# Performance work log

Hardware: AMD Instinct MI355X
Metric: run time of the kernel (lower is better)

Reference implementation:

```python
import jax, jax.numpy as jnp
import numpy as np

N = 50000
E = 800000
IN = 256
HID = 64
H12 = 4
LAT = 32
NEG_SLOPE = 0.2


def gat_conv(x, src, dst, W, a_src, a_dst, b, heads, out_ch, concat):
    """PyG GATConv (eval mode, add_self_loops already applied to src/dst).
    x: [N, F_in]; src/dst: [Etot]; W: [F_in, heads*out_ch]; a_*: [heads, out_ch]; b: bias.
    Returns (out, alpha[Etot, heads])."""
    n = x.shape[0]
    h = (x @ W).reshape(n, heads, out_ch)                 # [N,H,C]
    e_src = (h * a_src).sum(-1)                           # [N,H]
    e_dst = (h * a_dst).sum(-1)                           # [N,H]
    e = jax.nn.leaky_relu(e_src[src] + e_dst[dst], NEG_SLOPE)   # [Etot,H]
    emax = jax.ops.segment_max(e, dst, num_segments=n)
    ee = jnp.exp(e - emax[dst])
    denom = jax.ops.segment_sum(ee, dst, num_segments=n)
    alpha = ee / (denom[dst] + 1e-16)                     # segment softmax over incoming edges
    msg = h[src] * alpha[:, :, None]                      # [Etot,H,C]
    out = jax.ops.segment_sum(msg, dst, num_segments=n)   # [N,H,C]
    out = out.reshape(n, heads * out_ch) if concat else out.mean(axis=1)
    return out + b, alpha


def setup_inputs() -> dict:
    key = jax.random.key(0)
    ks = jax.random.split(key, 20)
    s = 0.1
    inp = {
        "x": jax.random.normal(ks[0], (N, IN), jnp.float32),
        "edge_index": jax.random.randint(ks[1], (2, E), 0, N, jnp.int32),
        "W1": jax.random.normal(ks[2], (IN, H12 * HID), jnp.float32) * s,
        "a1s": jax.random.normal(ks[3], (H12, HID), jnp.float32) * s,
        "a1d": jax.random.normal(ks[4], (H12, HID), jnp.float32) * s,
        "b1": jnp.zeros((H12 * HID,), jnp.float32),
        "W2": jax.random.normal(ks[5], (H12 * HID, H12 * HID), jnp.float32) * s,
        "a2s": jax.random.normal(ks[6], (H12, HID), jnp.float32) * s,
        "a2d": jax.random.normal(ks[7], (H12, HID), jnp.float32) * s,
        "b2": jnp.zeros((HID,), jnp.float32),
        "Wm": jax.random.normal(ks[8], (HID, LAT), jnp.float32) * s,
        "ams": jax.random.normal(ks[9], (1, LAT), jnp.float32) * s,
        "amd": jax.random.normal(ks[10], (1, LAT), jnp.float32) * s,
        "bm": jnp.zeros((LAT,), jnp.float32),
        # log_std head
        "Ws": jax.random.normal(ks[11], (HID, LAT), jnp.float32) * s,
        "ass": jax.random.normal(ks[12], (1, LAT), jnp.float32) * s,
        "asd": jax.random.normal(ks[13], (1, LAT), jnp.float32) * s,
        "bs": jnp.zeros((LAT,), jnp.float32),
    }
    return inp


def reference(x, edge_index, W1, a1s, a1d, b1, W2, a2s, a2d, b2,
              Wm, ams, amd, bm, Ws, ass, asd, bs):
    # GATConv adds self loops by default
    loops = jnp.arange(N, dtype=edge_index.dtype)
    src = jnp.concatenate([edge_index[0], loops])
    dst = jnp.concatenate([edge_index[1], loops])

    h1, a_w1 = gat_conv(x, src, dst, W1, a1s, a1d, b1, H12, HID, True)
    h1 = jax.nn.relu(h1)
    h2, a_w2 = gat_conv(h1, src, dst, W2, a2s, a2d, b2, H12, HID, False)
    h2 = jax.nn.relu(h2)  # dropout is identity in eval mode
    z_mean, a_wm = gat_conv(h2, src, dst, Wm, ams, amd, bm, 1, LAT, False)
    z_log_std, a_ws = gat_conv(h2, src, dst, Ws, ass, asd, bs, 1, LAT, False)
    return (z_mean, z_log_std, a_w1, a_w2, a_wm, a_ws)
```

## Files before the change

kernel.cpp:

```cpp
#include <hip/hip_runtime.h>
#include <cstdint>
#include <cstddef>

#define NN 50000
#define EE 800000
#define ETOT 850000
#define NEG_SLOPE 0.2f

typedef _Float16 f16;
typedef __attribute__((ext_vector_type(4))) _Float16 f16x4;
typedef __attribute__((ext_vector_type(8))) _Float16 f16x8;
typedef __attribute__((ext_vector_type(4))) float f32x4;


__global__ __launch_bounds__(256) void deg_kernel(const int* __restrict__ ei, int* __restrict__ deg) {
    int e = blockIdx.x * 256 + threadIdx.x;
    if (e >= ETOT) return;
    int d = (e < EE) ? ei[EE + e] : (e - EE);
    atomicAdd(&deg[d], 1);
}

__global__ __launch_bounds__(256) void scan1_kernel(const int* __restrict__ deg, int* __restrict__ offs,
                                                    int* __restrict__ bsum, int n) {
    __shared__ int sh[256];
    int i = blockIdx.x * 256 + threadIdx.x;
    int v = (i < n) ? deg[i] : 0;
    sh[threadIdx.x] = v;
    __syncthreads();
    for (int off = 1; off < 256; off <<= 1) {
        int t = (threadIdx.x >= off) ? sh[threadIdx.x - off] : 0;
        __syncthreads();
        sh[threadIdx.x] += t;
        __syncthreads();
    }
    if (i < n) offs[i] = sh[threadIdx.x] - v;
    if (threadIdx.x == 255) bsum[blockIdx.x] = sh[255];
}

__global__ __launch_bounds__(256) void scan2_kernel(int* __restrict__ bsum, int nb) {
    __shared__ int sh[256];
    int v = (threadIdx.x < nb) ? bsum[threadIdx.x] : 0;
    sh[threadIdx.x] = v;
    __syncthreads();
    for (int off = 1; off < 256; off <<= 1) {
        int t = (threadIdx.x >= off) ? sh[threadIdx.x - off] : 0;
        __syncthreads();
        sh[threadIdx.x] += t;
        __syncthreads();
    }
    if (threadIdx.x < nb) bsum[threadIdx.x] = sh[threadIdx.x] - v;
}

__global__ __launch_bounds__(256) void scan3_kernel(const int* __restrict__ bsum, int* __restrict__ offs,
                                                    int* __restrict__ cursor, int n) {
    int i = blockIdx.x * 256 + threadIdx.x;
    if (i < n) {
        int o = offs[i] + bsum[blockIdx.x];
        offs[i] = o;
        cursor[i] = o;
    }
}

__global__ __launch_bounds__(256) void fill_kernel(const int* __restrict__ ei, int* __restrict__ cursor,
                                                   int* __restrict__ csrc) {
    int e = blockIdx.x * 256 + threadIdx.x;
    if (e >= ETOT) return;
    int d, s;
    if (e < EE) { s = ei[e]; d = ei[EE + e]; } else { s = e - EE; d = e - EE; }
    int p = atomicAdd(&cursor[d], 1);
    csrc[p] = s;
}


template<int K, bool AF32>
__global__ __launch_bounds__(256) void mfma_gemm(const void* __restrict__ Ap, const f16* __restrict__ Bt,
                                                 f16* __restrict__ C, int M, int N) {
    int w = threadIdx.x >> 6, lane = threadIdx.x & 63;
    int m0 = blockIdx.y * 128 + w * 32;
    int n0 = blockIdx.x * 64;
    int r = lane & 15, kb = lane >> 4;
    int ar0 = m0 + r;       if (ar0 > M - 1) ar0 = M - 1;
    int ar1 = m0 + 16 + r;  if (ar1 > M - 1) ar1 = M - 1;
    f32x4 acc[2][4] = {};
    const float* Af = (const float*)Ap;
    const f16*   Ah = (const f16*)Ap;
    size_t a0off = (size_t)ar0 * K + kb * 8;
    size_t a1off = (size_t)ar1 * K + kb * 8;
    const f16* bbase = Bt + (size_t)(n0 + r) * K + kb * 8;
    for (int k0 = 0; k0 < K; k0 += 32) {
        f16x8 a0, a1;
        if constexpr (AF32) {
            float4 l0 = *(const float4*)(Af + a0off + k0);
            float4 h0 = *(const float4*)(Af + a0off + k0 + 4);
            float4 l1 = *(const float4*)(Af + a1off + k0);
            float4 h1 = *(const float4*)(Af + a1off + k0 + 4);
            a0[0]=(f16)l0.x; a0[1]=(f16)l0.y; a0[2]=(f16)l0.z; a0[3]=(f16)l0.w;
            a0[4]=(f16)h0.x; a0[5]=(f16)h0.y; a0[6]=(f16)h0.z; a0[7]=(f16)h0.w;
            a1[0]=(f16)l1.x; a1[1]=(f16)l1.y; a1[2]=(f16)l1.z; a1[3]=(f16)l1.w;
            a1[4]=(f16)h1.x; a1[5]=(f16)h1.y; a1[6]=(f16)h1.z; a1[7]=(f16)h1.w;
        } else {
            a0 = *(const f16x8*)(Ah + a0off + k0);
            a1 = *(const f16x8*)(Ah + a1off + k0);
        }
#pragma unroll
        for (int ni = 0; ni < 4; ++ni) {
            f16x8 b = *(const f16x8*)(bbase + (size_t)ni * 16 * K + k0);
            acc[0][ni] = __builtin_amdgcn_mfma_f32_16x16x32_f16(a0, b, acc[0][ni], 0, 0, 0);
            acc[1][ni] = __builtin_amdgcn_mfma_f32_16x16x32_f16(a1, b, acc[1][ni], 0, 0, 0);
        }
    }
#pragma unroll
    for (int mi = 0; mi < 2; ++mi) {
#pragma unroll
        for (int i = 0; i < 4; ++i) {
            int row = m0 + mi * 16 + kb * 4 + i;
            if (row < M) {
#pragma unroll
                for (int ni = 0; ni < 4; ++ni)
                    C[(size_t)row * N + n0 + ni * 16 + r] = (f16)acc[mi][ni][i];
            }
        }
    }
}


__global__ __launch_bounds__(256) void packw_kernel(const float* __restrict__ W1, const float* __restrict__ W2,
                                                    const float* __restrict__ Wm, const float* __restrict__ Ws,
                                                    const float* __restrict__ ams, const float* __restrict__ ass,
                                                    const float* __restrict__ amd, const float* __restrict__ asd,
                                                    f16* __restrict__ Wt1, f16* __restrict__ Wt2,
                                                    f16* __restrict__ Wtms,
                                                    float* __restrict__ aS, float* __restrict__ aD) {
    int i = blockIdx.x * 256 + threadIdx.x;
    if (i < 65536) {
        int n = i >> 8, k = i & 255;
        Wt1[(size_t)n * 256 + k] = (f16)W1[(size_t)k * 256 + n];
        Wt2[(size_t)n * 256 + k] = (f16)W2[(size_t)k * 256 + n];
    }
    if (i < 4096) {
        int c = i >> 6, k = i & 63;
        float v = (c < 32) ? Wm[k * 32 + c] : Ws[k * 32 + (c - 32)];
        Wtms[(size_t)c * 64 + k] = (f16)v;
    }
    if (i < 64) {
        aS[i] = (i < 32) ? ams[i] : ass[i - 32];
        aD[i] = (i < 32) ? amd[i] : asd[i - 32];
    }
}


__global__ __launch_bounds__(256) void scores4_kernel(const f16* __restrict__ H, const float* __restrict__ aS,
                                                      const float* __restrict__ aD, float* __restrict__ es,
                                                      float* __restrict__ ed) {
    int wave = threadIdx.x >> 6, lane = threadIdx.x & 63;
    int n = blockIdx.x * 4 + wave;
    if (n >= NN) return;
    f16x4 h = *(const f16x4*)(H + (size_t)n * 256 + lane * 4);
    float4 s4 = *(const float4*)(aS + lane * 4);
    float4 d4 = *(const float4*)(aD + lane * 4);
    float hx = (float)h[0], hy = (float)h[1], hz = (float)h[2], hw = (float)h[3];
    float ps = hx * s4.x + hy * s4.y + hz * s4.z + hw * s4.w;
    float pd = hx * d4.x + hy * d4.y + hz * d4.z + hw * d4.w;
    for (int off = 1; off < 16; off <<= 1) { ps += __shfl_xor(ps, off); pd += __shfl_xor(pd, off); }
    if ((lane & 15) == 0) {
        int hh = lane >> 4;
        es[n * 4 + hh] = ps;
        ed[n * 4 + hh] = pd;
    }
}

__global__ __launch_bounds__(256) void scores_ms_kernel(const f16* __restrict__ H, const float* __restrict__ aS,
                                                        const float* __restrict__ aD, float* __restrict__ es,
                                                        float* __restrict__ ed) {
    int wave = threadIdx.x >> 6, lane = threadIdx.x & 63;
    int n = blockIdx.x * 4 + wave;
    if (n >= NN) return;
    float h = (float)H[(size_t)n * 64 + lane];
    float ps = h * aS[lane];
    float pd = h * aD[lane];
    for (int off = 1; off < 32; off <<= 1) { ps += __shfl_xor(ps, off); pd += __shfl_xor(pd, off); }
    if ((lane & 31) == 0) {
        int g = lane >> 5;
        es[n * 2 + g] = ps;
        ed[n * 2 + g] = pd;
    }
}

__device__ __forceinline__ float leaky(float v) { return v > 0.f ? v : NEG_SLOPE * v; }


__global__ __launch_bounds__(256) void alpha4_kernel(const int* __restrict__ ei, const float* __restrict__ es,
                                                     const float* __restrict__ ed, const float* __restrict__ inv,
                                                     float* __restrict__ out4) {
    int e = blockIdx.x * 256 + threadIdx.x;
    if (e >= ETOT) return;
    int s, d;
    if (e < EE) { s = ei[e]; d = ei[EE + e]; } else { s = e - EE; d = e - EE; }
    float4 esv = *(const float4*)(es + (size_t)s * 4);
    float4 edv = *(const float4*)(ed + (size_t)d * 4);
    float4 iv  = *(const float4*)(inv + (size_t)d * 4);
    float4 r;
    r.x = __expf(leaky(esv.x + edv.x)) * iv.x;
    r.y = __expf(leaky(esv.y + edv.y)) * iv.y;
    r.z = __expf(leaky(esv.z + edv.z)) * iv.z;
    r.w = __expf(leaky(esv.w + edv.w)) * iv.w;
    *(float4*)(out4 + (size_t)e * 4) = r;
}

__global__ __launch_bounds__(256) void alpha_ms_kernel(const int* __restrict__ ei, const float* __restrict__ es,
                                                       const float* __restrict__ ed, const float* __restrict__ inv,
                                                       float* __restrict__ awm, float* __restrict__ aws) {
    int e = blockIdx.x * 256 + threadIdx.x;
    if (e >= ETOT) return;
    int s, d;
    if (e < EE) { s = ei[e]; d = ei[EE + e]; } else { s = e - EE; d = e - EE; }
    float2 esv = *(const float2*)(es + (size_t)s * 2);
    float2 edv = *(const float2*)(ed + (size_t)d * 2);
    float2 iv  = *(const float2*)(inv + (size_t)d * 2);
    awm[e] = __expf(leaky(esv.x + edv.x)) * iv.x;
    aws[e] = __expf(leaky(esv.y + edv.y)) * iv.y;
}


__global__ __launch_bounds__(128) void agg_concat_kernel(
    const f16* __restrict__ H, const float* __restrict__ es, const float* __restrict__ ed,
    const int* __restrict__ offs, const int* __restrict__ csrc,
    const float* __restrict__ bias, f16* __restrict__ out, float* __restrict__ invout) {
    int wave = threadIdx.x >> 6, lane = threadIdx.x & 63;
    int n = blockIdx.x * 2 + wave;
    if (n >= NN) return;
    int start = offs[n];
    int end = (n + 1 < NN) ? offs[n + 1] : ETOT;
    int deg = end - start;
    int h16 = lane >> 4, sub = lane & 15;
    float edh = ed[n * 4 + h16];
    float dsum = 0.f;
    for (int j = sub; j < deg; j += 16) {
        int s = csrc[start + j];
        dsum += __expf(leaky(es[s * 4 + h16] + edh));
    }
    for (int off = 1; off < 16; off <<= 1) dsum += __shfl_xor(dsum, off);
    float inv = 1.f / (dsum + 1e-16f);
    if (sub == 0) invout[n * 4 + h16] = inv;
    int half = lane >> 5;
    int l5 = lane & 31;
    int hh = l5 >> 3;
    int c8 = l5 * 8;
    float invh = __shfl(inv, hh << 4);
    float edhh = __shfl(edh, hh << 4);
    float accv[8] = {};
    int j = half;
    for (; j + 6 < deg; j += 8) {
        int p0 = start + j, p1 = start + j + 2, p2 = start + j + 4, p3 = start + j + 6;
        int s0 = csrc[p0], s1 = csrc[p1], s2 = csrc[p2], s3 = csrc[p3];
        float a0 = __expf(leaky(es[s0 * 4 + hh] + edhh)) * invh;
        float a1 = __expf(leaky(es[s1 * 4 + hh] + edhh)) * invh;
        float a2 = __expf(leaky(es[s2 * 4 + hh] + edhh)) * invh;
        float a3 = __expf(leaky(es[s3 * 4 + hh] + edhh)) * invh;
        f16x8 v0 = *(const f16x8*)(H + (size_t)s0 * 256 + c8);
        f16x8 v1 = *(const f16x8*)(H + (size_t)s1 * 256 + c8);
        f16x8 v2 = *(const f16x8*)(H + (size_t)s2 * 256 + c8);
        f16x8 v3 = *(const f16x8*)(H + (size_t)s3 * 256 + c8);
#pragma unroll
        for (int k = 0; k < 8; ++k)
            accv[k] += a0 * (float)v0[k] + a1 * (float)v1[k] + a2 * (float)v2[k] + a3 * (float)v3[k];
    }
    for (; j < deg; j += 2) {
        int p0 = start + j;
        int s0 = csrc[p0];
        float a0 = __expf(leaky(es[s0 * 4 + hh] + edhh)) * invh;
        f16x8 v0 = *(const f16x8*)(H + (size_t)s0 * 256 + c8);
#pragma unroll
        for (int k = 0; k < 8; ++k) accv[k] += a0 * (float)v0[k];
    }
#pragma unroll
    for (int k = 0; k < 8; ++k) accv[k] += __shfl_xor(accv[k], 32);
    if (lane < 32) {
        f16x8 r;
#pragma unroll
        for (int k = 0; k < 8; ++k) r[k] = (f16)fmaxf(accv[k] + bias[c8 + k], 0.f);
        *(f16x8*)(out + (size_t)n * 256 + c8) = r;
    }
}


__global__ __launch_bounds__(128) void agg_mean_kernel(
    const f16* __restrict__ H, const float* __restrict__ es, const float* __restrict__ ed,
    const int* __restrict__ offs, const int* __restrict__ csrc,
    const float* __restrict__ bias, f16* __restrict__ out, float* __restrict__ invout) {
    int wave = threadIdx.x >> 6, lane = threadIdx.x & 63;
    int n = blockIdx.x * 2 + wave;
    if (n >= NN) return;
    int start = offs[n];
    int end = (n + 1 < NN) ? offs[n + 1] : ETOT;
    int deg = end - start;
    int h16 = lane >> 4, sub = lane & 15;
    float edh = ed[n * 4 + h16];
    float dsum = 0.f;
    for (int j = sub; j < deg; j += 16) {
        int s = csrc[start + j];
        dsum += __expf(leaky(es[s * 4 + h16] + edh));
    }
    for (int off = 1; off < 16; off <<= 1) dsum += __shfl_xor(dsum, off);
    float inv = 1.f / (dsum + 1e-16f);
    if (sub == 0) invout[n * 4 + h16] = inv;
    int half = lane >> 5;
    int l5 = lane & 31;
    int hh = l5 >> 3;
    int c8 = l5 * 8;
    float invh = __shfl(inv, hh << 4);
    float edhh = __shfl(edh, hh << 4);
    float accv[8] = {};
    int j = half;
    for (; j + 6 < deg; j += 8) {
        int p0 = start + j, p1 = start + j + 2, p2 = start + j + 4, p3 = start + j + 6;
        int s0 = csrc[p0], s1 = csrc[p1], s2 = csrc[p2], s3 = csrc[p3];
        float a0 = __expf(leaky(es[s0 * 4 + hh] + edhh)) * invh;
        float a1 = __expf(leaky(es[s1 * 4 + hh] + edhh)) * invh;
        float a2 = __expf(leaky(es[s2 * 4 + hh] + edhh)) * invh;
        float a3 = __expf(leaky(es[s3 * 4 + hh] + edhh)) * invh;
        f16x8 v0 = *(const f16x8*)(H + (size_t)s0 * 256 + c8);
        f16x8 v1 = *(const f16x8*)(H + (size_t)s1 * 256 + c8);
        f16x8 v2 = *(const f16x8*)(H + (size_t)s2 * 256 + c8);
        f16x8 v3 = *(const f16x8*)(H + (size_t)s3 * 256 + c8);
#pragma unroll
        for (int k = 0; k < 8; ++k)
            accv[k] += a0 * (float)v0[k] + a1 * (float)v1[k] + a2 * (float)v2[k] + a3 * (float)v3[k];
    }
    for (; j < deg; j += 2) {
        int p0 = start + j;
        int s0 = csrc[p0];
        float a0 = __expf(leaky(es[s0 * 4 + hh] + edhh)) * invh;
        f16x8 v0 = *(const f16x8*)(H + (size_t)s0 * 256 + c8);
#pragma unroll
        for (int k = 0; k < 8; ++k) accv[k] += a0 * (float)v0[k];
    }
#pragma unroll
    for (int k = 0; k < 8; ++k) {
        accv[k] += __shfl_xor(accv[k], 8);
        accv[k] += __shfl_xor(accv[k], 16);
        accv[k] += __shfl_xor(accv[k], 32);
    }
    if (lane < 8) {
        f16x8 r;
#pragma unroll
        for (int k = 0; k < 8; ++k) r[k] = (f16)fmaxf(accv[k] * 0.25f + bias[lane * 8 + k], 0.f);
        *(f16x8*)(out + (size_t)n * 64 + lane * 8) = r;
    }
}


__global__ __launch_bounds__(128) void agg_ms_kernel(
    const f16* __restrict__ H, const float* __restrict__ es, const float* __restrict__ ed,
    const int* __restrict__ offs, const int* __restrict__ csrc,
    const float* __restrict__ bm, const float* __restrict__ bs,
    float* __restrict__ zmean, float* __restrict__ zlog, float* __restrict__ invout) {
    int wave = threadIdx.x >> 6, lane = threadIdx.x & 63;
    int n = blockIdx.x * 2 + wave;
    if (n >= NN) return;
    int start = offs[n];
    int end = (n + 1 < NN) ? offs[n + 1] : ETOT;
    int deg = end - start;
    int g = lane >> 5, sub = lane & 31;
    float edg = ed[n * 2 + g];
    float dsum = 0.f;
    for (int j = sub; j < deg; j += 32) {
        int s = csrc[start + j];
        dsum += __expf(leaky(es[s * 2 + g] + edg));
    }
    for (int off = 1; off < 32; off <<= 1) dsum += __shfl_xor(dsum, off);
    float inv = 1.f / (dsum + 1e-16f);
    if (sub == 0) invout[n * 2 + g] = inv;
    int slot = lane >> 3;
    int le = lane & 7;
    int g2 = le >> 2;
    int c8 = le * 8;
    float invg = __shfl(inv, g2 << 5);
    float edg2 = __shfl(edg, g2 << 5);
    float accv[8] = {};
    for (int j = slot; j < deg; j += 8) {
        int p = start + j;
        int s = csrc[p];
        float a = __expf(leaky(es[s * 2 + g2] + edg2)) * invg;
        f16x8 v = *(const f16x8*)(H + (size_t)s * 64 + c8);
#pragma unroll
        for (int k = 0; k < 8; ++k) accv[k] += a * (float)v[k];
    }
#pragma unroll
    for (int k = 0; k < 8; ++k) {
        accv[k] += __shfl_xor(accv[k], 8);
        accv[k] += __shfl_xor(accv[k], 16);
        accv[k] += __shfl_xor(accv[k], 32);
    }
    if (lane < 4) {
        float4 r0, r1;
        int cb = lane * 8;
        r0.x = accv[0] + bm[cb + 0]; r0.y = accv[1] + bm[cb + 1];
        r0.z = accv[2] + bm[cb + 2]; r0.w = accv[3] + bm[cb + 3];
        r1.x = accv[4] + bm[cb + 4]; r1.y = accv[5] + bm[cb + 5];
        r1.z = accv[6] + bm[cb + 6]; r1.w = accv[7] + bm[cb + 7];
        *(float4*)(zmean + (size_t)n * 32 + cb) = r0;
        *(float4*)(zmean + (size_t)n * 32 + cb + 4) = r1;
    } else if (lane < 8) {
        float4 r0, r1;
        int cb = (lane - 4) * 8;
        r0.x = accv[0] + bs[cb + 0]; r0.y = accv[1] + bs[cb + 1];
        r0.z = accv[2] + bs[cb + 2]; r0.w = accv[3] + bs[cb + 3];
        r1.x = accv[4] + bs[cb + 4]; r1.y = accv[5] + bs[cb + 5];
        r1.z = accv[6] + bs[cb + 6]; r1.w = accv[7] + bs[cb + 7];
        *(float4*)(zlog + (size_t)n * 32 + cb) = r0;
        *(float4*)(zlog + (size_t)n * 32 + cb + 4) = r1;
    }
}


extern "C" void kernel_launch(void* const* d_in, const int* in_sizes, int n_in,
                              void* d_out, int out_size, void* d_ws, size_t ws_size,
                              hipStream_t stream) {
    const float* x   = (const float*)d_in[0];
    const int*   ei  = (const int*)d_in[1];
    const float* W1  = (const float*)d_in[2];
    const float* a1s = (const float*)d_in[3];
    const float* a1d = (const float*)d_in[4];
    const float* b1  = (const float*)d_in[5];
    const float* W2  = (const float*)d_in[6];
    const float* a2s = (const float*)d_in[7];
    const float* a2d = (const float*)d_in[8];
    const float* b2  = (const float*)d_in[9];
    const float* Wm  = (const float*)d_in[10];
    const float* ams = (const float*)d_in[11];
    const float* amd = (const float*)d_in[12];
    const float* bm  = (const float*)d_in[13];
    const float* Ws  = (const float*)d_in[14];
    const float* ass = (const float*)d_in[15];
    const float* asd = (const float*)d_in[16];
    const float* bs  = (const float*)d_in[17];

    float* out = (float*)d_out;
    float* zmean = out;
    float* zlog  = out + 1600000;
    float* a_w1  = out + 3200000;
    float* a_w2  = out + 6600000;
    float* a_wm  = out + 10000000;
    float* a_ws_o = out + 10850000;

    float* ws = (float*)d_ws;
    size_t o = 0;
    f16*   Hh   = (f16*)(ws + o); o += (size_t)NN * 128;
    f16*   h1h  = (f16*)(ws + o); o += (size_t)NN * 128;
    f16*   h2h  = (f16*)(ws + o); o += (size_t)NN * 32;
    float* es1  = ws + o; o += NN * 4;
    float* ed1  = ws + o; o += NN * 4;
    float* es2  = ws + o; o += NN * 4;
    float* ed2  = ws + o; o += NN * 4;
    float* esms = ws + o; o += NN * 2;
    float* edms = ws + o; o += NN * 2;
    float* inv1 = ws + o; o += NN * 4;
    float* inv2 = ws + o; o += NN * 4;
    float* invms= ws + o; o += NN * 2;
    f16*   Wt1  = (f16*)(ws + o); o += 32768;
    f16*   Wt2  = (f16*)(ws + o); o += 32768;
    f16*   Wtms = (f16*)(ws + o); o += 2048;
    float* aSms = ws + o; o += 64;
    float* aDms = ws + o; o += 64;
    int* deg    = (int*)(ws + o); o += NN;
    int* offs   = (int*)(ws + o); o += NN;
    int* cursor = (int*)(ws + o); o += NN;
    int* csrc   = (int*)(ws + o); o += ETOT;

    const int edgeBlocks = (ETOT + 255) / 256;
    const int nodeBlocks = (NN + 255) / 256;
    const int waveBlocks = (NN + 3) / 4;
    const int aggBlocks  = (NN + 1) / 2;

    hipMemsetAsync(deg, 0, NN * sizeof(int), stream);
    deg_kernel<<<edgeBlocks, 256, 0, stream>>>(ei, deg);
    scan1_kernel<<<nodeBlocks, 256, 0, stream>>>(deg, offs, cursor , NN);
    scan2_kernel<<<1, 256, 0, stream>>>(cursor, nodeBlocks);
    scan3_kernel<<<nodeBlocks, 256, 0, stream>>>(cursor, offs, deg , NN);
    fill_kernel<<<edgeBlocks, 256, 0, stream>>>(ei, deg, csrc);

    packw_kernel<<<256, 256, 0, stream>>>(W1, W2, Wm, Ws, ams, ass, amd, asd, Wt1, Wt2, Wtms, aSms, aDms);

    dim3 gg1(4, (NN + 127) / 128);
    dim3 gg3(1, (NN + 127) / 128);
    mfma_gemm<256, true><<<gg1, 256, 0, stream>>>(x, Wt1, Hh, NN, 256);
    scores4_kernel<<<waveBlocks, 256, 0, stream>>>(Hh, a1s, a1d, es1, ed1);
    agg_concat_kernel<<<aggBlocks, 128, 0, stream>>>(Hh, es1, ed1, offs, csrc, b1, h1h, inv1);
    alpha4_kernel<<<edgeBlocks, 256, 0, stream>>>(ei, es1, ed1, inv1, a_w1);

    mfma_gemm<256, false><<<gg1, 256, 0, stream>>>(h1h, Wt2, Hh, NN, 256);
    scores4_kernel<<<waveBlocks, 256, 0, stream>>>(Hh, a2s, a2d, es2, ed2);
    agg_mean_kernel<<<aggBlocks, 128, 0, stream>>>(Hh, es2, ed2, offs, csrc, b2, h2h, inv2);
    alpha4_kernel<<<edgeBlocks, 256, 0, stream>>>(ei, es2, ed2, inv2, a_w2);

    mfma_gemm<64, false><<<gg3, 256, 0, stream>>>(h2h, Wtms, Hh, NN, 64);
    scores_ms_kernel<<<waveBlocks, 256, 0, stream>>>(Hh, aSms, aDms, esms, edms);
    agg_ms_kernel<<<aggBlocks, 128, 0, stream>>>(Hh, esms, edms, offs, csrc, bm, bs,
                                                 zmean, zlog, invms);
    alpha_ms_kernel<<<edgeBlocks, 256, 0, stream>>>(ei, esms, edms, invms, a_wm, a_ws_o);
}
```

Before: 544.0 us.

## Fuse attention score computation into GEMM epilogue and deepen gather unrolling

The GEMM kernel is restructured so each block computes all output columns for 64 rows, keeping the A rows in registers. The per-head attention scores are reduced straight from the accumulators in the epilogue, which removes the separate scores kernels and their re-read of H. The aggregation kernels also unroll their neighbour gathers more deeply (8 loads in flight instead of 4) to raise memory-level parallelism. The cost is more registers, possibly lower occupancy, and B being re-read per block with less reuse across M.

```diff
diff --git a/kernel.cpp b/kernel.cpp
--- a/kernel.cpp
+++ b/kernel.cpp
@@ -72,52 +72,88 @@
 }
 
 
-template<int K, bool AF32>
-__global__ __launch_bounds__(256) void mfma_gemm(const void* __restrict__ Ap, const f16* __restrict__ Bt,
-                                                 f16* __restrict__ C, int M, int N) {
+template<int K, int NCB, int NH, bool AF32>
+__global__ __launch_bounds__(256) void mfma_gemm_fused(
+    const void* __restrict__ Ap, const f16* __restrict__ Bt, f16* __restrict__ C,
+    const float* __restrict__ aS, const float* __restrict__ aD,
+    float* __restrict__ es, float* __restrict__ ed, int M) {
+    constexpr int N = NCB * 64;
     int w = threadIdx.x >> 6, lane = threadIdx.x & 63;
-    int m0 = blockIdx.y * 128 + w * 32;
-    int n0 = blockIdx.x * 64;
+    int m0 = blockIdx.x * 64 + w * 16;
     int r = lane & 15, kb = lane >> 4;
-    int ar0 = m0 + r;       if (ar0 > M - 1) ar0 = M - 1;
-    int ar1 = m0 + 16 + r;  if (ar1 > M - 1) ar1 = M - 1;
-    f32x4 acc[2][4] = {};
+    int ar = m0 + r; if (ar > M - 1) ar = M - 1;
     const float* Af = (const float*)Ap;
     const f16*   Ah = (const f16*)Ap;
-    size_t a0off = (size_t)ar0 * K + kb * 8;
-    size_t a1off = (size_t)ar1 * K + kb * 8;
-    const f16* bbase = Bt + (size_t)(n0 + r) * K + kb * 8;
-    for (int k0 = 0; k0 < K; k0 += 32) {
-        f16x8 a0, a1;
+    f16x8 a[K / 32];
+    size_t aoff = (size_t)ar * K + kb * 8;
+#pragma unroll
+    for (int ks = 0; ks < K / 32; ++ks) {
         if constexpr (AF32) {
-            float4 l0 = *(const float4*)(Af + a0off + k0);
-            float4 h0 = *(const float4*)(Af + a0off + k0 + 4);
-            float4 l1 = *(const float4*)(Af + a1off + k0);
-            float4 h1 = *(const float4*)(Af + a1off + k0 + 4);
-            a0[0]=(f16)l0.x; a0[1]=(f16)l0.y; a0[2]=(f16)l0.z; a0[3]=(f16)l0.w;
-            a0[4]=(f16)h0.x; a0[5]=(f16)h0.y; a0[6]=(f16)h0.z; a0[7]=(f16)h0.w;
-            a1[0]=(f16)l1.x; a1[1]=(f16)l1.y; a1[2]=(f16)l1.z; a1[3]=(f16)l1.w;
-            a1[4]=(f16)h1.x; a1[5]=(f16)h1.y; a1[6]=(f16)h1.z; a1[7]=(f16)h1.w;
+            float4 l0 = *(const float4*)(Af + aoff + ks * 32);
+            float4 h0 = *(const float4*)(Af + aoff + ks * 32 + 4);
+            a[ks][0] = (f16)l0.x; a[ks][1] = (f16)l0.y; a[ks][2] = (f16)l0.z; a[ks][3] = (f16)l0.w;
+            a[ks][4] = (f16)h0.x; a[ks][5] = (f16)h0.y; a[ks][6] = (f16)h0.z; a[ks][7] = (f16)h0.w;
         } else {
-            a0 = *(const f16x8*)(Ah + a0off + k0);
-            a1 = *(const f16x8*)(Ah + a1off + k0);
+            a[ks] = *(const f16x8*)(Ah + aoff + ks * 32);
         }
+    }
+#pragma unroll
+    for (int cb = 0; cb < NCB; ++cb) {
+        f32x4 acc[4] = {};
+        const f16* bbase = Bt + (size_t)(cb * 64 + r) * K + kb * 8;
+#pragma unroll
+        for (int ks = 0; ks < K / 32; ++ks) {
+#pragma unroll
+            for (int ni = 0; ni < 4; ++ni) {
+                f16x8 b = *(const f16x8*)(bbase + (size_t)ni * 16 * K + ks * 32);
+                acc[ni] = __builtin_amdgcn_mfma_f32_16x16x32_f16(a[ks], b, acc[ni], 0, 0, 0);
+            }
+        }
+        float aSl[4], aDl[4];
 #pragma unroll
         for (int ni = 0; ni < 4; ++ni) {
-            f16x8 b = *(const f16x8*)(bbase + (size_t)ni * 16 * K + k0);
-            acc[0][ni] = __builtin_amdgcn_mfma_f32_16x16x32_f16(a0, b, acc[0][ni], 0, 0, 0);
-            acc[1][ni] = __builtin_amdgcn_mfma_f32_16x16x32_f16(a1, b, acc[1][ni], 0, 0, 0);
+            aSl[ni] = aS[cb * 64 + ni * 16 + r];
+            aDl[ni] = aD[cb * 64 + ni * 16 + r];
         }
-    }
-#pragma unroll
-    for (int mi = 0; mi < 2; ++mi) {
 #pragma unroll
         for (int i = 0; i < 4; ++i) {
-            int row = m0 + mi * 16 + kb * 4 + i;
-            if (row < M) {
+            int row = m0 + kb * 4 + i;
+            bool ok = row < M;
+            if (ok) {
 #pragma unroll
                 for (int ni = 0; ni < 4; ++ni)
-                    C[(size_t)row * N + n0 + ni * 16 + r] = (f16)acc[mi][ni][i];
+                    C[(size_t)row * N + cb * 64 + ni * 16 + r] = (f16)acc[ni][i];
+            }
+            if constexpr (NH == 4) {
+                float pes = acc[0][i] * aSl[0] + acc[1][i] * aSl[1] + acc[2][i] * aSl[2] + acc[3][i] * aSl[3];
+                float ped = acc[0][i] * aDl[0] + acc[1][i] * aDl[1] + acc[2][i] * aDl[2] + acc[3][i] * aDl[3];
+#pragma unroll
+                for (int off = 1; off < 16; off <<= 1) {
+                    pes += __shfl_xor(pes, off);
+                    ped += __shfl_xor(ped, off);
+                }
+                if (r == 0 && ok) {
+                    es[(size_t)row * 4 + cb] = pes;
+                    ed[(size_t)row * 4 + cb] = ped;
+                }
+            } else {
+                float p0s = acc[0][i] * aSl[0] + acc[1][i] * aSl[1];
+                float p1s = acc[2][i] * aSl[2] + acc[3][i] * aSl[3];
+                float p0d = acc[0][i] * aDl[0] + acc[1][i] * aDl[1];
+                float p1d = acc[2][i] * aDl[2] + acc[3][i] * aDl[3];
+#pragma unroll
+                for (int off = 1; off < 16; off <<= 1) {
+                    p0s += __shfl_xor(p0s, off);
+                    p1s += __shfl_xor(p1s, off);
+                    p0d += __shfl_xor(p0d, off);
+                    p1d += __shfl_xor(p1d, off);
+                }
+                if (r == 0 && ok) {
+                    es[(size_t)row * 2 + 0] = p0s;
+                    es[(size_t)row * 2 + 1] = p1s;
+                    ed[(size_t)row * 2 + 0] = p0d;
+                    ed[(size_t)row * 2 + 1] = p1d;
+                }
             }
         }
     }
@@ -145,44 +181,6 @@
     if (i < 64) {
         aS[i] = (i < 32) ? ams[i] : ass[i - 32];
         aD[i] = (i < 32) ? amd[i] : asd[i - 32];
-    }
-}
-
-
-__global__ __launch_bounds__(256) void scores4_kernel(const f16* __restrict__ H, const float* __restrict__ aS,
-                                                      const float* __restrict__ aD, float* __restrict__ es,
-                                                      float* __restrict__ ed) {
-    int wave = threadIdx.x >> 6, lane = threadIdx.x & 63;
-    int n = blockIdx.x * 4 + wave;
-    if (n >= NN) return;
-    f16x4 h = *(const f16x4*)(H + (size_t)n * 256 + lane * 4);
-    float4 s4 = *(const float4*)(aS + lane * 4);
-    float4 d4 = *(const float4*)(aD + lane * 4);
-    float hx = (float)h[0], hy = (float)h[1], hz = (float)h[2], hw = (float)h[3];
-    float ps = hx * s4.x + hy * s4.y + hz * s4.z + hw * s4.w;
-    float pd = hx * d4.x + hy * d4.y + hz * d4.z + hw * d4.w;
-    for (int off = 1; off < 16; off <<= 1) { ps += __shfl_xor(ps, off); pd += __shfl_xor(pd, off); }
-    if ((lane & 15) == 0) {
-        int hh = lane >> 4;
-        es[n * 4 + hh] = ps;
-        ed[n * 4 + hh] = pd;
-    }
-}
-
-__global__ __launch_bounds__(256) void scores_ms_kernel(const f16* __restrict__ H, const float* __restrict__ aS,
-                                                        const float* __restrict__ aD, float* __restrict__ es,
-                                                        float* __restrict__ ed) {
-    int wave = threadIdx.x >> 6, lane = threadIdx.x & 63;
-    int n = blockIdx.x * 4 + wave;
-    if (n >= NN) return;
-    float h = (float)H[(size_t)n * 64 + lane];
-    float ps = h * aS[lane];
-    float pd = h * aD[lane];
-    for (int off = 1; off < 32; off <<= 1) { ps += __shfl_xor(ps, off); pd += __shfl_xor(pd, off); }
-    if ((lane & 31) == 0) {
-        int g = lane >> 5;
-        es[n * 2 + g] = ps;
-        ed[n * 2 + g] = pd;
     }
 }
 
@@ -250,24 +248,24 @@
     float edhh = __shfl(edh, hh << 4);
     float accv[8] = {};
     int j = half;
-    for (; j + 6 < deg; j += 8) {
-        int p0 = start + j, p1 = start + j + 2, p2 = start + j + 4, p3 = start + j + 6;
-        int s0 = csrc[p0], s1 = csrc[p1], s2 = csrc[p2], s3 = csrc[p3];
-        float a0 = __expf(leaky(es[s0 * 4 + hh] + edhh)) * invh;
-        float a1 = __expf(leaky(es[s1 * 4 + hh] + edhh)) * invh;
-        float a2 = __expf(leaky(es[s2 * 4 + hh] + edhh)) * invh;
-        float a3 = __expf(leaky(es[s3 * 4 + hh] + edhh)) * invh;
-        f16x8 v0 = *(const f16x8*)(H + (size_t)s0 * 256 + c8);
-        f16x8 v1 = *(const f16x8*)(H + (size_t)s1 * 256 + c8);
-        f16x8 v2 = *(const f16x8*)(H + (size_t)s2 * 256 + c8);
-        f16x8 v3 = *(const f16x8*)(H + (size_t)s3 * 256 + c8);
-#pragma unroll
-        for (int k = 0; k < 8; ++k)
-            accv[k] += a0 * (float)v0[k] + a1 * (float)v1[k] + a2 * (float)v2[k] + a3 * (float)v3[k];
+    for (; j + 14 < deg; j += 16) {
+        int s[8];
+#pragma unroll
+        for (int t = 0; t < 8; ++t) s[t] = csrc[start + j + 2 * t];
+        f16x8 v[8];
+#pragma unroll
+        for (int t = 0; t < 8; ++t) v[t] = *(const f16x8*)(H + (size_t)s[t] * 256 + c8);
+        float av[8];
+#pragma unroll
+        for (int t = 0; t < 8; ++t) av[t] = __expf(leaky(es[s[t] * 4 + hh] + edhh)) * invh;
+#pragma unroll
+        for (int t = 0; t < 8; ++t) {
+#pragma unroll
+            for (int k = 0; k < 8; ++k) accv[k] += av[t] * (float)v[t][k];
+        }
     }
     for (; j < deg; j += 2) {
-        int p0 = start + j;
-        int s0 = csrc[p0];
+        int s0 = csrc[start + j];
         float a0 = __expf(leaky(es[s0 * 4 + hh] + edhh)) * invh;
         f16x8 v0 = *(const f16x8*)(H + (size_t)s0 * 256 + c8);
 #pragma unroll
@@ -312,24 +310,24 @@
     float edhh = __shfl(edh, hh << 4);
     float accv[8] = {};
     int j = half;
-    for (; j + 6 < deg; j += 8) {
-        int p0 = start + j, p1 = start + j + 2, p2 = start + j + 4, p3 = start + j + 6;
-        int s0 = csrc[p0], s1 = csrc[p1], s2 = csrc[p2], s3 = csrc[p3];
-        float a0 = __expf(leaky(es[s0 * 4 + hh] + edhh)) * invh;
-        float a1 = __expf(leaky(es[s1 * 4 + hh] + edhh)) * invh;
-        float a2 = __expf(leaky(es[s2 * 4 + hh] + edhh)) * invh;
-        float a3 = __expf(leaky(es[s3 * 4 + hh] + edhh)) * invh;
-        f16x8 v0 = *(const f16x8*)(H + (size_t)s0 * 256 + c8);
-        f16x8 v1 = *(const f16x8*)(H + (size_t)s1 * 256 + c8);
-        f16x8 v2 = *(const f16x8*)(H + (size_t)s2 * 256 + c8);
-        f16x8 v3 = *(const f16x8*)(H + (size_t)s3 * 256 + c8);
-#pragma unroll
-        for (int k = 0; k < 8; ++k)
-            accv[k] += a0 * (float)v0[k] + a1 * (float)v1[k] + a2 * (float)v2[k] + a3 * (float)v3[k];
+    for (; j + 14 < deg; j += 16) {
+        int s[8];
+#pragma unroll
+        for (int t = 0; t < 8; ++t) s[t] = csrc[start + j + 2 * t];
+        f16x8 v[8];
+#pragma unroll
+        for (int t = 0; t < 8; ++t) v[t] = *(const f16x8*)(H + (size_t)s[t] * 256 + c8);
+        float av[8];
+#pragma unroll
+        for (int t = 0; t < 8; ++t) av[t] = __expf(leaky(es[s[t] * 4 + hh] + edhh)) * invh;
+#pragma unroll
+        for (int t = 0; t < 8; ++t) {
+#pragma unroll
+            for (int k = 0; k < 8; ++k) accv[k] += av[t] * (float)v[t][k];
+        }
     }
     for (; j < deg; j += 2) {
-        int p0 = start + j;
-        int s0 = csrc[p0];
+        int s0 = csrc[start + j];
         float a0 = __expf(leaky(es[s0 * 4 + hh] + edhh)) * invh;
         f16x8 v0 = *(const f16x8*)(H + (size_t)s0 * 256 + c8);
 #pragma unroll
@@ -378,9 +376,19 @@
     float invg = __shfl(inv, g2 << 5);
     float edg2 = __shfl(edg, g2 << 5);
     float accv[8] = {};
-    for (int j = slot; j < deg; j += 8) {
-        int p = start + j;
-        int s = csrc[p];
+    int j = slot;
+    for (; j + 8 < deg; j += 16) {
+        int s0 = csrc[start + j];
+        int s1 = csrc[start + j + 8];
+        f16x8 v0 = *(const f16x8*)(H + (size_t)s0 * 64 + c8);
+        f16x8 v1 = *(const f16x8*)(H + (size_t)s1 * 64 + c8);
+        float a0 = __expf(leaky(es[s0 * 2 + g2] + edg2)) * invg;
+        float a1 = __expf(leaky(es[s1 * 2 + g2] + edg2)) * invg;
+#pragma unroll
+        for (int k = 0; k < 8; ++k) accv[k] += a0 * (float)v0[k] + a1 * (float)v1[k];
+    }
+    for (; j < deg; j += 8) {
+        int s = csrc[start + j];
         float a = __expf(leaky(es[s * 2 + g2] + edg2)) * invg;
         f16x8 v = *(const f16x8*)(H + (size_t)s * 64 + c8);
 #pragma unroll
@@ -470,8 +478,8 @@
 
     const int edgeBlocks = (ETOT + 255) / 256;
     const int nodeBlocks = (NN + 255) / 256;
-    const int waveBlocks = (NN + 3) / 4;
     const int aggBlocks  = (NN + 1) / 2;
+    const int gemmBlocks = (NN + 63) / 64;
 
     hipMemsetAsync(deg, 0, NN * sizeof(int), stream);
     deg_kernel<<<edgeBlocks, 256, 0, stream>>>(ei, deg);
@@ -482,20 +490,15 @@
 
     packw_kernel<<<256, 256, 0, stream>>>(W1, W2, Wm, Ws, ams, ass, amd, asd, Wt1, Wt2, Wtms, aSms, aDms);
 
-    dim3 gg1(4, (NN + 127) / 128);
-    dim3 gg3(1, (NN + 127) / 128);
-    mfma_gemm<256, true><<<gg1, 256, 0, stream>>>(x, Wt1, Hh, NN, 256);
-    scores4_kernel<<<waveBlocks, 256, 0, stream>>>(Hh, a1s, a1d, es1, ed1);
+    mfma_gemm_fused<256, 4, 4, true><<<gemmBlocks, 256, 0, stream>>>(x, Wt1, Hh, a1s, a1d, es1, ed1, NN);
     agg_concat_kernel<<<aggBlocks, 128, 0, stream>>>(Hh, es1, ed1, offs, csrc, b1, h1h, inv1);
     alpha4_kernel<<<edgeBlocks, 256, 0, stream>>>(ei, es1, ed1, inv1, a_w1);
 
-    mfma_gemm<256, false><<<gg1, 256, 0, stream>>>(h1h, Wt2, Hh, NN, 256);
-    scores4_kernel<<<waveBlocks, 256, 0, stream>>>(Hh, a2s, a2d, es2, ed2);
+    mfma_gemm_fused<256, 4, 4, false><<<gemmBlocks, 256, 0, stream>>>(h1h, Wt2, Hh, a2s, a2d, es2, ed2, NN);
     agg_mean_kernel<<<aggBlocks, 128, 0, stream>>>(Hh, es2, ed2, offs, csrc, b2, h2h, inv2);
     alpha4_kernel<<<edgeBlocks, 256, 0, stream>>>(ei, es2, ed2, inv2, a_w2);
 
-    mfma_gemm<64, false><<<gg3, 256, 0, stream>>>(h2h, Wtms, Hh, NN, 64);
-    scores_ms_kernel<<<waveBlocks, 256, 0, stream>>>(Hh, aSms, aDms, esms, edms);
+    mfma_gemm_fused<64, 1, 2, false><<<gemmBlocks, 256, 0, stream>>>(h2h, Wtms, Hh, aSms, aDms, esms, edms, NN);
     agg_ms_kernel<<<aggBlocks, 128, 0, stream>>>(Hh, esms, edms, offs, csrc, bm, bs,
                                                  zmean, zlog, invms);
     alpha_ms_kernel<<<edgeBlocks, 256, 0, stream>>>(ei, esms, edms, invms, a_wm, a_ws_o);
```

After: 608.8 us. 11.9% more time.
